# Kernel optimization log

Measured on AMD Instinct MI355X. Metric: run time of the kernel, lower is better.

The kernel has to match this reference:

```python
import jax, jax.numpy as jnp
import numpy as np
from jax import lax

NUM_UNITS = 128
INPUT_DIM = 128
NUM_STEPS = 512
BATCH = 256
FORGET_BIAS = 1.0  # BasicLSTMCell(num_units, 1.0)


def setup_inputs() -> dict:
    key = jax.random.key(0)
    k1, k2 = jax.random.split(key)
    x = jax.random.normal(k1, (BATCH, NUM_STEPS, INPUT_DIM), dtype=jnp.float32)
    # BasicLSTMCell kernel: [input_dim + num_units, 4*num_units], gate order i, j, f, o
    W = jax.random.normal(k2, (INPUT_DIM + NUM_UNITS, 4 * NUM_UNITS), dtype=jnp.float32) * 0.05
    b = jnp.zeros((4 * NUM_UNITS,), dtype=jnp.float32)  # zeros init in TF
    return {"x": x, "W": W, "b": b}


def reference(x, W, b):
    # x: [B, T, D]; faithful BasicLSTMCell recurrence, return_sequences=True
    B = x.shape[0]
    U = NUM_UNITS

    def step(carry, xt):
        c, h = carry
        gates = jnp.concatenate([xt, h], axis=-1) @ W + b  # [B, 4U]
        i, j, f, o = jnp.split(gates, 4, axis=-1)
        new_c = c * jax.nn.sigmoid(f + FORGET_BIAS) + jax.nn.sigmoid(i) * jnp.tanh(j)
        new_h = jnp.tanh(new_c) * jax.nn.sigmoid(o)
        return (new_c, new_h), new_h

    init = (jnp.zeros((B, U), x.dtype), jnp.zeros((B, U), x.dtype))
    _, hs = lax.scan(step, init, jnp.swapaxes(x, 0, 1))  # hs: [T, B, U]
    return jnp.swapaxes(hs, 0, 1)  # [B, T, U]
```

## Files before the change

### kernel.cpp

```cpp
#include <hip/hip_runtime.h>
#include <cstdint>

#define B_ 256
#define T_ 512
#define D_ 128
#define U_ 128

typedef _Float16 h2_t __attribute__((ext_vector_type(2)));
typedef _Float16 f16x4 __attribute__((ext_vector_type(4)));
typedef _Float16 f16x8 __attribute__((ext_vector_type(8)));
typedef float f32x4 __attribute__((ext_vector_type(4)));

static __device__ __forceinline__ uint32_t pack2(float a, float b) {
  h2_t h;
  h.x = (_Float16)a;
  h.y = (_Float16)b;
  return __builtin_bit_cast(uint32_t, h);
}
static __device__ __forceinline__ h2_t as_h2(uint32_t u) {
  return __builtin_bit_cast(h2_t, u);
}
static __device__ __forceinline__ float dot2acc(uint32_t a, uint32_t w, float acc) {
#if __has_builtin(__builtin_amdgcn_fdot2)
  return __builtin_amdgcn_fdot2(as_h2(a), as_h2(w), acc, false);
#else
  h2_t ha = as_h2(a), hw = as_h2(w);
  return acc + (float)ha.x * (float)hw.x + (float)ha.y * (float)hw.y;
#endif
}

static __device__ __forceinline__ float fexp2(float x) {
#if __has_builtin(__builtin_amdgcn_exp2f)
  return __builtin_amdgcn_exp2f(x);
#else
  return __exp2f(x);
#endif
}
static __device__ __forceinline__ float frcp(float x) {
#if __has_builtin(__builtin_amdgcn_rcpf)
  return __builtin_amdgcn_rcpf(x);
#else
  return __frcp_rn(x);
#endif
}
#define LOG2E_ 1.44269504f
static __device__ __forceinline__ float sigm(float v) {
  return frcp(1.0f + fexp2(-LOG2E_ * v));
}
static __device__ __forceinline__ float tanh_(float v) {
  float r = frcp(1.0f + fexp2(-2.0f * LOG2E_ * v));
  return __builtin_fmaf(2.0f, r, -1.0f);
}

__global__ __launch_bounds__(256) void wt_kernel(const float* __restrict__ W,
                                                 _Float16* __restrict__ Wtx,
                                                 _Float16* __restrict__ Wth) {
  int id = blockIdx.x * 256 + threadIdx.x;
  int col = id >> 8, k = id & 255;
  _Float16 v = (_Float16)W[(size_t)k * 512 + col];
  if (k < 128) Wtx[col * 128 + k] = v;
  else Wth[col * 128 + (k - 128)] = v;
}

__global__ __launch_bounds__(256, 2) void gx_kernel(const float* __restrict__ x,
                                                    const _Float16* __restrict__ Wt,
                                                    const float* __restrict__ bias,
                                                    _Float16* __restrict__ gx) {
  __shared__ __align__(16) _Float16 As[64 * 136];
  const int tid = threadIdx.x;
  const int w = tid >> 6, l = tid & 63;
  const size_t rowBase = (size_t)blockIdx.x * 64;

  const float4* xs = reinterpret_cast<const float4*>(x + rowBase * 128);
#pragma unroll
  for (int n = 0; n < 8; ++n) {
    int idx4 = tid + 256 * n;
    float4 v = xs[idx4];
    int f = idx4 * 4;
    int r = f >> 7, cc = f & 127;
    f16x4 p;
    p.x = (_Float16)v.x; p.y = (_Float16)v.y;
    p.z = (_Float16)v.z; p.w = (_Float16)v.w;
    *reinterpret_cast<f16x4*>(&As[r * 136 + cc]) = p;
  }
  __syncthreads();

  f16x8 af[4][4];
#pragma unroll
  for (int rt = 0; rt < 4; ++rt)
#pragma unroll
    for (int kk = 0; kk < 4; ++kk)
      af[rt][kk] = *reinterpret_cast<const f16x8*>(
          &As[(16 * rt + (l & 15)) * 136 + 32 * kk + 8 * (l >> 4)]);

  const int colBase = 128 * w;
#pragma unroll 1
  for (int ct = 0; ct < 8; ++ct) {
    const int col = colBase + 16 * ct + (l & 15);
    const float bb = bias[col] + ((col >= 256 && col < 384) ? 1.0f : 0.0f);
    f32x4 acc[4];
#pragma unroll
    for (int rt = 0; rt < 4; ++rt) acc[rt] = (f32x4){0.f, 0.f, 0.f, 0.f};
    const _Float16* wtc = Wt + (size_t)col * 128 + 8 * (l >> 4);
#pragma unroll
    for (int kk = 0; kk < 4; ++kk) {
      f16x8 bf = *reinterpret_cast<const f16x8*>(wtc + 32 * kk);
#pragma unroll
      for (int rt = 0; rt < 4; ++rt)
        acc[rt] = __builtin_amdgcn_mfma_f32_16x16x32_f16(af[rt][kk], bf, acc[rt], 0, 0, 0);
    }
    const int u = col & 127, g = col >> 7;
#pragma unroll
    for (int rt = 0; rt < 4; ++rt) {
      size_t row = rowBase + 16 * rt + 4 * (l >> 4);
#pragma unroll
      for (int j = 0; j < 4; ++j)
        gx[(row + j) * 512 + u * 4 + g] = (_Float16)(acc[rt][j] + bb);
    }
  }
}

__global__ __launch_bounds__(512, 1) void rec_kernel(
    const _Float16* __restrict__ Wth,
    const uint16_t* __restrict__ gx2,
    float* __restrict__ out) {
  __shared__ __align__(16) _Float16 hbuf[2][4][128];
  const int tid = threadIdx.x;
  const int b = blockIdx.x;
  const int w = tid >> 6, l = tid & 63;
  const int lq = l >> 4;
  const int u = 16 * w + (l & 15);
  const bool wr = (lq == 0);

  f16x8 bw[4][4];
#pragma unroll
  for (int g = 0; g < 4; ++g) {
    const _Float16* wc = Wth + (size_t)(128 * g + u) * 128 + 8 * lq;
#pragma unroll
    for (int kk = 0; kk < 4; ++kk)
      bw[g][kk] = *reinterpret_cast<const f16x8*>(wc + 32 * kk);
  }
#pragma unroll
  for (int g = 0; g < 4; ++g)
#pragma unroll
    for (int kk = 0; kk < 4; ++kk)
      asm volatile("" : "+a"(bw[g][kk]));

  const uint16_t* gxb = gx2 + (size_t)b * T_ * 512 + 4 * u;
  float* ob = out + (size_t)b * T_ * U_ + u;

  reinterpret_cast<uint32_t*>(&hbuf[0][0][0])[tid] = 0u;

  f32x4 Z = {0.f, 0.f, 0.f, 0.f};
  asm volatile("" : "+v"(Z));
  float cst = 0.0f;

#define GXLD(idx) \
  (*reinterpret_cast<const f16x4*>(gxb + (size_t)((idx) < T_ ? (idx) : (T_ - 1)) * 512))

  f16x4 gp0 = GXLD(0), gp1 = GXLD(1), gp2 = GXLD(2), gp3 = GXLD(3);
  __syncthreads();

#define MFMA_INIT(d, a, bfr)                                  \
  asm("v_mfma_f32_16x16x32_f16 %0, %1, %2, %3"                \
      : "=v"(d) : "v"(a), "a"(bfr), "v"(Z))
#define MFMA_ACC(d, a, bfr)                                   \
  asm("v_mfma_f32_16x16x32_f16 %0, %1, %2, %0"                \
      : "+v"(d) : "v"(a), "a"(bfr))

#define LDS_BARRIER()                                                  \
  do {                                                                 \
    asm volatile("s_waitcnt lgkmcnt(0)\n\ts_barrier" ::: "memory");    \
    __builtin_amdgcn_sched_barrier(0);                                 \
  } while (0)

#define STEP(tt, p, gv)                                                        \
  {                                                                            \
    const _Float16* hb = &hbuf[p][lq][0];                                      \
    f16x8 a0 = *reinterpret_cast<const f16x8*>(hb + 8 * lq);                   \
    f16x8 a1 = *reinterpret_cast<const f16x8*>(hb + 32 + 8 * lq);              \
    f16x8 a2 = *reinterpret_cast<const f16x8*>(hb + 64 + 8 * lq);              \
    f16x8 a3 = *reinterpret_cast<const f16x8*>(hb + 96 + 8 * lq);              \
    f32x4 c0, c1, c2, c3, d0, d1, d2, d3;                                      \
    MFMA_INIT(c0, a0, bw[0][0]);                                               \
    MFMA_INIT(c1, a0, bw[1][0]);                                               \
    MFMA_INIT(c2, a0, bw[2][0]);                                               \
    MFMA_INIT(c3, a0, bw[3][0]);                                               \
    MFMA_INIT(d0, a2, bw[0][2]);                                               \
    MFMA_INIT(d1, a2, bw[1][2]);                                               \
    MFMA_INIT(d2, a2, bw[2][2]);                                               \
    MFMA_INIT(d3, a2, bw[3][2]);                                               \
    MFMA_ACC(c0, a1, bw[0][1]);                                                \
    MFMA_ACC(c1, a1, bw[1][1]);                                                \
    MFMA_ACC(c2, a1, bw[2][1]);                                                \
    MFMA_ACC(c3, a1, bw[3][1]);                                                \
    MFMA_ACC(d0, a3, bw[0][3]);                                                \
    MFMA_ACC(d1, a3, bw[1][3]);                                                \
    MFMA_ACC(d2, a3, bw[2][3]);                                                \
    MFMA_ACC(d3, a3, bw[3][3]);                                                \
         \
    asm volatile("s_nop 7\n\ts_nop 7"                                          \
                 : "+v"(c0), "+v"(c1), "+v"(c2), "+v"(c3),                     \
                   "+v"(d0), "+v"(d1), "+v"(d2), "+v"(d3));                    \
    const float gi = (c0[0] + d0[0]) + (float)(gv).x;                          \
    const float gj = (c1[0] + d1[0]) + (float)(gv).y;                          \
    const float gf = (c2[0] + d2[0]) + (float)(gv).z;                          \
    const float go = (c3[0] + d3[0]) + (float)(gv).w;                          \
    cst = __builtin_fmaf(cst, sigm(gf), sigm(gi) * tanh_(gj));                 \
    const float hh = tanh_(cst) * sigm(go);                                    \
    hbuf[(p) ^ 1][lq][u] = (_Float16)hh;                                       \
    if (wr) ob[(size_t)(tt) * U_] = hh;                                        \
    LDS_BARRIER();                                                             \
  }

#pragma unroll 1
  for (int t = 0; t < T_; t += 4) {
    STEP(t + 0, 0, gp0)
    gp0 = GXLD(t + 4);
    STEP(t + 1, 1, gp1)
    gp1 = GXLD(t + 5);
    STEP(t + 2, 0, gp2)
    gp2 = GXLD(t + 6);
    STEP(t + 3, 1, gp3)
    gp3 = GXLD(t + 7);
  }
#undef STEP
#undef MFMA_INIT
#undef MFMA_ACC
#undef LDS_BARRIER
#undef GXLD
}

__global__ __launch_bounds__(512, 2) void lstm_fused_kernel(
    const float* __restrict__ x, const float* __restrict__ W,
    const float* __restrict__ bias, float* __restrict__ out) {
  __shared__ __align__(16) uint32_t a_lds[2][128];
  __shared__ float g_lds[512];
  const int tid = threadIdx.x;
  const int b = blockIdx.x;
  uint32_t wreg[128];
#pragma unroll
  for (int q4 = 0; q4 < 32; ++q4) {
    float f[8];
#pragma unroll
    for (int r = 0; r < 8; ++r) f[r] = W[(q4 * 8 + r) * 512 + tid];
#pragma unroll
    for (int rr = 0; rr < 4; ++rr)
      wreg[q4 * 4 + rr] = pack2(f[2 * rr], f[2 * rr + 1]);
  }
  const float bjv = bias[tid];
  const float* xb = x + (size_t)b * (T_ * D_);
  float* ob = out + (size_t)b * (T_ * U_);
  if (tid < 32) {
    float4 x4 = reinterpret_cast<const float4*>(xb)[tid];
    reinterpret_cast<uint2*>(&a_lds[0][0])[tid] =
        make_uint2(pack2(x4.x, x4.y), pack2(x4.z, x4.w));
  }
  if (tid >= 64 && tid < 128) a_lds[0][tid] = 0u;
  __syncthreads();
  float c = 0.0f;
  int p = 0;
  for (int t = 0; t < T_; ++t) {
    float4 xp;
    const bool pf = (tid < 32) && (t + 1 < T_);
    if (pf) xp = reinterpret_cast<const float4*>(xb + (t + 1) * D_)[tid];
    const uint4* av = reinterpret_cast<const uint4*>(&a_lds[p][0]);
    float a0 = bjv, a1 = 0.0f, a2 = 0.0f, a3 = 0.0f;
#pragma unroll
    for (int q = 0; q < 32; ++q) {
      uint4 a4 = av[q];
      a0 = dot2acc(a4.x, wreg[4 * q + 0], a0);
      a1 = dot2acc(a4.y, wreg[4 * q + 1], a1);
      a2 = dot2acc(a4.z, wreg[4 * q + 2], a2);
      a3 = dot2acc(a4.w, wreg[4 * q + 3], a3);
    }
    g_lds[tid] = (a0 + a1) + (a2 + a3);
    __syncthreads();
    if (tid < 128) {
      const float gi = g_lds[tid];
      const float gj = g_lds[128 + tid];
      const float gf = g_lds[256 + tid];
      const float go = g_lds[384 + tid];
      c = c * sigm(gf + 1.0f) + sigm(gi) * tanh_(gj);
      const float h = tanh_(c) * sigm(go);
      ob[t * U_ + tid] = h;
      reinterpret_cast<_Float16*>(&a_lds[p ^ 1][64])[tid] = (_Float16)h;
    }
    if (pf) {
      reinterpret_cast<uint2*>(&a_lds[p ^ 1][0])[tid] =
          make_uint2(pack2(xp.x, xp.y), pack2(xp.z, xp.w));
    }
    __syncthreads();
    p ^= 1;
  }
}

extern "C" void kernel_launch(void* const* d_in, const int* in_sizes, int n_in,
                              void* d_out, int out_size, void* d_ws, size_t ws_size,
                              hipStream_t stream) {
  (void)in_sizes; (void)n_in; (void)out_size;
  const float* x = (const float*)d_in[0];
  const float* W = (const float*)d_in[1];
  const float* b = (const float*)d_in[2];
  float* out = (float*)d_out;

  const size_t WTX_BYTES = (size_t)512 * 128 * 2;
  const size_t WTH_BYTES = (size_t)512 * 128 * 2;
  const size_t GX_BYTES = (size_t)B_ * T_ * 512 * 2;
  if (ws_size >= WTX_BYTES + WTH_BYTES + GX_BYTES) {
    _Float16* wtx = (_Float16*)d_ws;
    _Float16* wth = (_Float16*)((char*)d_ws + WTX_BYTES);
    _Float16* gxp = (_Float16*)((char*)d_ws + WTX_BYTES + WTH_BYTES);
    wt_kernel<<<512, 256, 0, stream>>>(W, wtx, wth);
    gx_kernel<<<2048, 256, 0, stream>>>(x, wtx, b, gxp);
    rec_kernel<<<256, 512, 0, stream>>>(wth, (const uint16_t*)gxp, out);
  } else {
    lstm_fused_kernel<<<256, 512, 0, stream>>>(x, W, b, out);
  }
}
```

Baseline: 305.9 us.

## Process four batch rows per recurrence block to cut grid from 256 to 64

The recurrent kernel now handles four batch elements per workgroup, one per lane quadrant, instead of one. Each step issues four sets of MFMAs over separate padded h buffers and picks each lane's gates with a select. This gives every lane useful output work and interleaves independent MFMA chains to hide latency. In exchange, each block does four times the MFMA work per step, and only 64 blocks run, which leaves most CUs idle.

```diff
diff --git a/kernel.cpp b/kernel.cpp
--- a/kernel.cpp
+++ b/kernel.cpp
@@ -50,6 +50,11 @@
 static __device__ __forceinline__ float tanh_(float v) {
   float r = frcp(1.0f + fexp2(-2.0f * LOG2E_ * v));
   return __builtin_fmaf(2.0f, r, -1.0f);
+}
+static __device__ __forceinline__ float sel4(float a, float b, float c, float d, int lq) {
+  float x = (lq & 1) ? b : a;
+  float y = (lq & 1) ? d : c;
+  return (lq & 2) ? y : x;
 }
 
 __global__ __launch_bounds__(256) void wt_kernel(const float* __restrict__ W,
@@ -124,13 +129,12 @@
     const _Float16* __restrict__ Wth,
     const uint16_t* __restrict__ gx2,
     float* __restrict__ out) {
-  __shared__ __align__(16) _Float16 hbuf[2][4][128];
+  __shared__ __align__(16) _Float16 hbuf[2][4 * 144];
   const int tid = threadIdx.x;
-  const int b = blockIdx.x;
   const int w = tid >> 6, l = tid & 63;
   const int lq = l >> 4;
   const int u = 16 * w + (l & 15);
-  const bool wr = (lq == 0);
+  const int b = blockIdx.x * 4 + lq;
 
   f16x8 bw[4][4];
 #pragma unroll
@@ -149,7 +153,8 @@
   const uint16_t* gxb = gx2 + (size_t)b * T_ * 512 + 4 * u;
   float* ob = out + (size_t)b * T_ * U_ + u;
 
-  reinterpret_cast<uint32_t*>(&hbuf[0][0][0])[tid] = 0u;
+  for (int i = tid; i < 576; i += 512)
+    reinterpret_cast<uint32_t*>(&hbuf[0][0])[i] = 0u;
 
   f32x4 Z = {0.f, 0.f, 0.f, 0.f};
   asm volatile("" : "+v"(Z));
@@ -158,14 +163,14 @@
 #define GXLD(idx) \
   (*reinterpret_cast<const f16x4*>(gxb + (size_t)((idx) < T_ ? (idx) : (T_ - 1)) * 512))
 
-  f16x4 gp0 = GXLD(0), gp1 = GXLD(1), gp2 = GXLD(2), gp3 = GXLD(3);
+  f16x4 gA = GXLD(0), gB = GXLD(1);
   __syncthreads();
 
-#define MFMA_INIT(d, a, bfr)                                  \
-  asm("v_mfma_f32_16x16x32_f16 %0, %1, %2, %3"                \
+#define MFMA_INIT(d, a, bfr)                    \
+  asm("v_mfma_f32_16x16x32_f16 %0, %1, %2, %3"  \
       : "=v"(d) : "v"(a), "a"(bfr), "v"(Z))
-#define MFMA_ACC(d, a, bfr)                                   \
-  asm("v_mfma_f32_16x16x32_f16 %0, %1, %2, %0"                \
+#define MFMA_ACC(d, a, bfr)                     \
+  asm("v_mfma_f32_16x16x32_f16 %0, %1, %2, %0"  \
       : "+v"(d) : "v"(a), "a"(bfr))
 
 #define LDS_BARRIER()                                                  \
@@ -174,60 +179,74 @@
     __builtin_amdgcn_sched_barrier(0);                                 \
   } while (0)
 
-#define STEP(tt, p, gv)                                                        \
+#define MF16(a0_, a1_, a2_, a3_, c0_, c1_, c2_, c3_, d0_, d1_, d2_, d3_) \
+  MFMA_INIT(c0_, a0_, bw[0][0]); MFMA_INIT(c1_, a0_, bw[1][0]);          \
+  MFMA_INIT(c2_, a0_, bw[2][0]); MFMA_INIT(c3_, a0_, bw[3][0]);          \
+  MFMA_INIT(d0_, a2_, bw[0][2]); MFMA_INIT(d1_, a2_, bw[1][2]);          \
+  MFMA_INIT(d2_, a2_, bw[2][2]); MFMA_INIT(d3_, a2_, bw[3][2]);          \
+  MFMA_ACC(c0_, a1_, bw[0][1]);  MFMA_ACC(c1_, a1_, bw[1][1]);           \
+  MFMA_ACC(c2_, a1_, bw[2][1]);  MFMA_ACC(c3_, a1_, bw[3][1]);           \
+  MFMA_ACC(d0_, a3_, bw[0][3]);  MFMA_ACC(d1_, a3_, bw[1][3]);           \
+  MFMA_ACC(d2_, a3_, bw[2][3]);  MFMA_ACC(d3_, a3_, bw[3][3]);
+
+#define EXTRACT(gi_, gj_, gf_, go_, c0_, c1_, c2_, c3_, d0_, d1_, d2_, d3_)    \
+  asm volatile("s_nop 7\n\ts_nop 7"                                            \
+               : "+v"(c0_), "+v"(c1_), "+v"(c2_), "+v"(c3_),                   \
+                 "+v"(d0_), "+v"(d1_), "+v"(d2_), "+v"(d3_));                  \
+  gi_ = c0_[0] + d0_[0]; gj_ = c1_[0] + d1_[0];                                \
+  gf_ = c2_[0] + d2_[0]; go_ = c3_[0] + d3_[0];
+
+#define LDH(hp, q, kk) \
+  (*reinterpret_cast<const f16x8*>((hp) + (q) * 144 + 32 * (kk) + 8 * lq))
+
+#define PERIOD(tt, p, gv)                                                      \
   {                                                                            \
-    const _Float16* hb = &hbuf[p][lq][0];                                      \
-    f16x8 a0 = *reinterpret_cast<const f16x8*>(hb + 8 * lq);                   \
-    f16x8 a1 = *reinterpret_cast<const f16x8*>(hb + 32 + 8 * lq);              \
-    f16x8 a2 = *reinterpret_cast<const f16x8*>(hb + 64 + 8 * lq);              \
-    f16x8 a3 = *reinterpret_cast<const f16x8*>(hb + 96 + 8 * lq);              \
-    f32x4 c0, c1, c2, c3, d0, d1, d2, d3;                                      \
-    MFMA_INIT(c0, a0, bw[0][0]);                                               \
-    MFMA_INIT(c1, a0, bw[1][0]);                                               \
-    MFMA_INIT(c2, a0, bw[2][0]);                                               \
-    MFMA_INIT(c3, a0, bw[3][0]);                                               \
-    MFMA_INIT(d0, a2, bw[0][2]);                                               \
-    MFMA_INIT(d1, a2, bw[1][2]);                                               \
-    MFMA_INIT(d2, a2, bw[2][2]);                                               \
-    MFMA_INIT(d3, a2, bw[3][2]);                                               \
-    MFMA_ACC(c0, a1, bw[0][1]);                                                \
-    MFMA_ACC(c1, a1, bw[1][1]);                                                \
-    MFMA_ACC(c2, a1, bw[2][1]);                                                \
-    MFMA_ACC(c3, a1, bw[3][1]);                                                \
-    MFMA_ACC(d0, a3, bw[0][3]);                                                \
-    MFMA_ACC(d1, a3, bw[1][3]);                                                \
-    MFMA_ACC(d2, a3, bw[2][3]);                                                \
-    MFMA_ACC(d3, a3, bw[3][3]);                                                \
-         \
-    asm volatile("s_nop 7\n\ts_nop 7"                                          \
-                 : "+v"(c0), "+v"(c1), "+v"(c2), "+v"(c3),                     \
-                   "+v"(d0), "+v"(d1), "+v"(d2), "+v"(d3));                    \
-    const float gi = (c0[0] + d0[0]) + (float)(gv).x;                          \
-    const float gj = (c1[0] + d1[0]) + (float)(gv).y;                          \
-    const float gf = (c2[0] + d2[0]) + (float)(gv).z;                          \
-    const float go = (c3[0] + d3[0]) + (float)(gv).w;                          \
+    const _Float16* hp = &hbuf[p][0];                                          \
+    f16x8 A00 = LDH(hp, 0, 0), A01 = LDH(hp, 0, 1),                            \
+          A02 = LDH(hp, 0, 2), A03 = LDH(hp, 0, 3);                            \
+    f16x8 A10 = LDH(hp, 1, 0), A11 = LDH(hp, 1, 1),                            \
+          A12 = LDH(hp, 1, 2), A13 = LDH(hp, 1, 3);                            \
+    f16x8 A20 = LDH(hp, 2, 0), A21 = LDH(hp, 2, 1),                            \
+          A22 = LDH(hp, 2, 2), A23 = LDH(hp, 2, 3);                            \
+    f16x8 A30 = LDH(hp, 3, 0), A31 = LDH(hp, 3, 1),                            \
+          A32 = LDH(hp, 3, 2), A33 = LDH(hp, 3, 3);                            \
+    f32x4 X0, X1, X2, X3, X4, X5, X6, X7;                                      \
+    f32x4 Y0, Y1, Y2, Y3, Y4, Y5, Y6, Y7;                                      \
+    float G0i, G0j, G0f, G0o, G1i, G1j, G1f, G1o;                              \
+    float G2i, G2j, G2f, G2o, G3i, G3j, G3f, G3o;                              \
+    MF16(A00, A01, A02, A03, X0, X1, X2, X3, X4, X5, X6, X7)                   \
+    MF16(A10, A11, A12, A13, Y0, Y1, Y2, Y3, Y4, Y5, Y6, Y7)                   \
+    EXTRACT(G0i, G0j, G0f, G0o, X0, X1, X2, X3, X4, X5, X6, X7)                \
+    MF16(A20, A21, A22, A23, X0, X1, X2, X3, X4, X5, X6, X7)                   \
+    EXTRACT(G1i, G1j, G1f, G1o, Y0, Y1, Y2, Y3, Y4, Y5, Y6, Y7)                \
+    MF16(A30, A31, A32, A33, Y0, Y1, Y2, Y3, Y4, Y5, Y6, Y7)                   \
+    EXTRACT(G2i, G2j, G2f, G2o, X0, X1, X2, X3, X4, X5, X6, X7)                \
+    EXTRACT(G3i, G3j, G3f, G3o, Y0, Y1, Y2, Y3, Y4, Y5, Y6, Y7)                \
+    float gi = sel4(G0i, G1i, G2i, G3i, lq) + (float)(gv).x;                   \
+    float gj = sel4(G0j, G1j, G2j, G3j, lq) + (float)(gv).y;                   \
+    float gf = sel4(G0f, G1f, G2f, G3f, lq) + (float)(gv).z;                   \
+    float go = sel4(G0o, G1o, G2o, G3o, lq) + (float)(gv).w;                   \
     cst = __builtin_fmaf(cst, sigm(gf), sigm(gi) * tanh_(gj));                 \
     const float hh = tanh_(cst) * sigm(go);                                    \
-    hbuf[(p) ^ 1][lq][u] = (_Float16)hh;                                       \
-    if (wr) ob[(size_t)(tt) * U_] = hh;                                        \
+    hbuf[(p) ^ 1][lq * 144 + u] = (_Float16)hh;                                \
+    ob[(size_t)(tt) * U_] = hh;                                                \
     LDS_BARRIER();                                                             \
   }
 
 #pragma unroll 1
-  for (int t = 0; t < T_; t += 4) {
-    STEP(t + 0, 0, gp0)
-    gp0 = GXLD(t + 4);
-    STEP(t + 1, 1, gp1)
-    gp1 = GXLD(t + 5);
-    STEP(t + 2, 0, gp2)
-    gp2 = GXLD(t + 6);
-    STEP(t + 3, 1, gp3)
-    gp3 = GXLD(t + 7);
-  }
-#undef STEP
+  for (int t = 0; t < T_; t += 2) {
+    PERIOD(t + 0, 0, gA)
+    gA = GXLD(t + 2);
+    PERIOD(t + 1, 1, gB)
+    gB = GXLD(t + 3);
+  }
+#undef PERIOD
+#undef LDH
+#undef EXTRACT
+#undef MF16
+#undef LDS_BARRIER
 #undef MFMA_INIT
 #undef MFMA_ACC
-#undef LDS_BARRIER
 #undef GXLD
 }
 
@@ -313,7 +332,7 @@
     _Float16* gxp = (_Float16*)((char*)d_ws + WTX_BYTES + WTH_BYTES);
     wt_kernel<<<512, 256, 0, stream>>>(W, wtx, wth);
     gx_kernel<<<2048, 256, 0, stream>>>(x, wtx, b, gxp);
-    rec_kernel<<<256, 512, 0, stream>>>(wth, (const uint16_t*)gxp, out);
+    rec_kernel<<<64, 512, 0, stream>>>(wth, (const uint16_t*)gxp, out);
   } else {
     lstm_fused_kernel<<<256, 512, 0, stream>>>(x, W, b, out);
   }
```

New measurement: 740.6 us. 142% more time.

## Halve recurrent block to 4 waves, each computing 32 units via 8 MFMA chains

Applied to the files above, without the earlier changes.

The recurrent kernel now runs 256 threads (4 waves) per batch row instead of 512. Each wave handles 32 hidden units, holding 8 weight fragment sets in AGPRs and issuing 32 MFMAs per step in 8 independent accumulation chains. The h buffer shrinks to a single shared row, and only the first quarter of each wave's lanes writes it. This cuts barrier participants and per-step LDS traffic, at the cost of longer per-wave MFMA chains and more register pressure on the serial critical path.

```diff
diff --git a/kernel.cpp b/kernel.cpp
--- a/kernel.cpp
+++ b/kernel.cpp
@@ -120,52 +120,59 @@
   }
 }
 
-__global__ __launch_bounds__(512, 1) void rec_kernel(
+__global__ __launch_bounds__(256, 1) void rec_kernel(
     const _Float16* __restrict__ Wth,
     const uint16_t* __restrict__ gx2,
     float* __restrict__ out) {
-  __shared__ __align__(16) _Float16 hbuf[2][4][128];
+  __shared__ __align__(16) _Float16 hbuf[2][128];
   const int tid = threadIdx.x;
   const int b = blockIdx.x;
   const int w = tid >> 6, l = tid & 63;
   const int lq = l >> 4;
-  const int u = 16 * w + (l & 15);
+  const int cI = l & 15;
   const bool wr = (lq == 0);
 
-  f16x8 bw[4][4];
-#pragma unroll
-  for (int g = 0; g < 4; ++g) {
-    const _Float16* wc = Wth + (size_t)(128 * g + u) * 128 + 8 * lq;
-#pragma unroll
-    for (int kk = 0; kk < 4; ++kk)
-      bw[g][kk] = *reinterpret_cast<const f16x8*>(wc + 32 * kk);
-  }
+  f16x8 bw[8][4];
 #pragma unroll
   for (int g = 0; g < 4; ++g)
 #pragma unroll
-    for (int kk = 0; kk < 4; ++kk)
-      asm volatile("" : "+a"(bw[g][kk]));
-
-  const uint16_t* gxb = gx2 + (size_t)b * T_ * 512 + 4 * u;
-  float* ob = out + (size_t)b * T_ * U_ + u;
-
-  reinterpret_cast<uint32_t*>(&hbuf[0][0][0])[tid] = 0u;
+    for (int s = 0; s < 2; ++s) {
+      const _Float16* wc =
+          Wth + (size_t)(128 * g + 32 * w + 16 * s + cI) * 128 + 8 * lq;
+#pragma unroll
+      for (int kt = 0; kt < 4; ++kt)
+        bw[g * 2 + s][kt] = *reinterpret_cast<const f16x8*>(wc + 32 * kt);
+    }
+#pragma unroll
+  for (int i = 0; i < 8; ++i)
+#pragma unroll
+    for (int kt = 0; kt < 4; ++kt)
+      asm volatile("" : "+a"(bw[i][kt]));
+
+  const int u0 = 32 * w + cI;
+  const uint16_t* gxb = gx2 + (size_t)b * T_ * 512 + 4 * u0;
+  float* ob = out + (size_t)b * T_ * U_ + u0;
+
+  if (tid < 128) reinterpret_cast<uint32_t*>(&hbuf[0][0])[tid] = 0u;
 
   f32x4 Z = {0.f, 0.f, 0.f, 0.f};
   asm volatile("" : "+v"(Z));
-  float cst = 0.0f;
-
-#define GXLD(idx) \
-  (*reinterpret_cast<const f16x4*>(gxb + (size_t)((idx) < T_ ? (idx) : (T_ - 1)) * 512))
-
-  f16x4 gp0 = GXLD(0), gp1 = GXLD(1), gp2 = GXLD(2), gp3 = GXLD(3);
+  float cst0 = 0.0f, cst1 = 0.0f;
+
+#define GXA(idx) (*reinterpret_cast<const f16x4*>( \
+    gxb + (size_t)((idx) < T_ ? (idx) : (T_ - 1)) * 512))
+#define GXB(idx) (*reinterpret_cast<const f16x4*>( \
+    gxb + (size_t)((idx) < T_ ? (idx) : (T_ - 1)) * 512 + 64))
+
+  f16x4 g0a = GXA(0), g0b = GXB(0), g1a = GXA(1), g1b = GXB(1);
+  f16x4 g2a = GXA(2), g2b = GXB(2), g3a = GXA(3), g3b = GXB(3);
   __syncthreads();
 
-#define MFMA_INIT(d, a, bfr)                                  \
-  asm("v_mfma_f32_16x16x32_f16 %0, %1, %2, %3"                \
+#define MFMA_INIT(d, a, bfr)                    \
+  asm("v_mfma_f32_16x16x32_f16 %0, %1, %2, %3"  \
       : "=v"(d) : "v"(a), "a"(bfr), "v"(Z))
-#define MFMA_ACC(d, a, bfr)                                   \
-  asm("v_mfma_f32_16x16x32_f16 %0, %1, %2, %0"                \
+#define MFMA_ACC(d, a, bfr)                     \
+  asm("v_mfma_f32_16x16x32_f16 %0, %1, %2, %0"  \
       : "+v"(d) : "v"(a), "a"(bfr))
 
 #define LDS_BARRIER()                                                  \
@@ -174,61 +181,72 @@
     __builtin_amdgcn_sched_barrier(0);                                 \
   } while (0)
 
-#define STEP(tt, p, gv)                                                        \
+#define STEP(tt, p, gva, gvb)                                                  \
   {                                                                            \
-    const _Float16* hb = &hbuf[p][lq][0];                                      \
+    const _Float16* hb = &hbuf[p][0];                                          \
     f16x8 a0 = *reinterpret_cast<const f16x8*>(hb + 8 * lq);                   \
     f16x8 a1 = *reinterpret_cast<const f16x8*>(hb + 32 + 8 * lq);              \
     f16x8 a2 = *reinterpret_cast<const f16x8*>(hb + 64 + 8 * lq);              \
     f16x8 a3 = *reinterpret_cast<const f16x8*>(hb + 96 + 8 * lq);              \
-    f32x4 c0, c1, c2, c3, d0, d1, d2, d3;                                      \
-    MFMA_INIT(c0, a0, bw[0][0]);                                               \
-    MFMA_INIT(c1, a0, bw[1][0]);                                               \
-    MFMA_INIT(c2, a0, bw[2][0]);                                               \
-    MFMA_INIT(c3, a0, bw[3][0]);                                               \
-    MFMA_INIT(d0, a2, bw[0][2]);                                               \
-    MFMA_INIT(d1, a2, bw[1][2]);                                               \
-    MFMA_INIT(d2, a2, bw[2][2]);                                               \
-    MFMA_INIT(d3, a2, bw[3][2]);                                               \
-    MFMA_ACC(c0, a1, bw[0][1]);                                                \
-    MFMA_ACC(c1, a1, bw[1][1]);                                                \
-    MFMA_ACC(c2, a1, bw[2][1]);                                                \
-    MFMA_ACC(c3, a1, bw[3][1]);                                                \
-    MFMA_ACC(d0, a3, bw[0][3]);                                                \
-    MFMA_ACC(d1, a3, bw[1][3]);                                                \
-    MFMA_ACC(d2, a3, bw[2][3]);                                                \
-    MFMA_ACC(d3, a3, bw[3][3]);                                                \
-         \
+    f32x4 q0, q1, q2, q3, q4, q5, q6, q7;                                      \
+    MFMA_INIT(q0, a0, bw[0][0]); MFMA_INIT(q1, a0, bw[1][0]);                  \
+    MFMA_INIT(q2, a0, bw[2][0]); MFMA_INIT(q3, a0, bw[3][0]);                  \
+    MFMA_INIT(q4, a0, bw[4][0]); MFMA_INIT(q5, a0, bw[5][0]);                  \
+    MFMA_INIT(q6, a0, bw[6][0]); MFMA_INIT(q7, a0, bw[7][0]);                  \
+    MFMA_ACC(q0, a1, bw[0][1]);  MFMA_ACC(q1, a1, bw[1][1]);                   \
+    MFMA_ACC(q2, a1, bw[2][1]);  MFMA_ACC(q3, a1, bw[3][1]);                   \
+    MFMA_ACC(q4, a1, bw[4][1]);  MFMA_ACC(q5, a1, bw[5][1]);                   \
+    MFMA_ACC(q6, a1, bw[6][1]);  MFMA_ACC(q7, a1, bw[7][1]);                   \
+    MFMA_ACC(q0, a2, bw[0][2]);  MFMA_ACC(q1, a2, bw[1][2]);                   \
+    MFMA_ACC(q2, a2, bw[2][2]);  MFMA_ACC(q3, a2, bw[3][2]);                   \
+    MFMA_ACC(q4, a2, bw[4][2]);  MFMA_ACC(q5, a2, bw[5][2]);                   \
+    MFMA_ACC(q6, a2, bw[6][2]);  MFMA_ACC(q7, a2, bw[7][2]);                   \
+    MFMA_ACC(q0, a3, bw[0][3]);  MFMA_ACC(q1, a3, bw[1][3]);                   \
+    MFMA_ACC(q2, a3, bw[2][3]);  MFMA_ACC(q3, a3, bw[3][3]);                   \
+    MFMA_ACC(q4, a3, bw[4][3]);  MFMA_ACC(q5, a3, bw[5][3]);                   \
+    MFMA_ACC(q6, a3, bw[6][3]);  MFMA_ACC(q7, a3, bw[7][3]);                   \
     asm volatile("s_nop 7\n\ts_nop 7"                                          \
-                 : "+v"(c0), "+v"(c1), "+v"(c2), "+v"(c3),                     \
-                   "+v"(d0), "+v"(d1), "+v"(d2), "+v"(d3));                    \
-    const float gi = (c0[0] + d0[0]) + (float)(gv).x;                          \
-    const float gj = (c1[0] + d1[0]) + (float)(gv).y;                          \
-    const float gf = (c2[0] + d2[0]) + (float)(gv).z;                          \
-    const float go = (c3[0] + d3[0]) + (float)(gv).w;                          \
-    cst = __builtin_fmaf(cst, sigm(gf), sigm(gi) * tanh_(gj));                 \
-    const float hh = tanh_(cst) * sigm(go);                                    \
-    hbuf[(p) ^ 1][lq][u] = (_Float16)hh;                                       \
-    if (wr) ob[(size_t)(tt) * U_] = hh;                                        \
+                 : "+v"(q0), "+v"(q1), "+v"(q2), "+v"(q3),                     \
+                   "+v"(q4), "+v"(q5), "+v"(q6), "+v"(q7));                    \
+        \
+    const float gi0 = q0[0] + (float)(gva).x;                                  \
+    const float gj0 = q2[0] + (float)(gva).y;                                  \
+    const float gf0 = q4[0] + (float)(gva).z;                                  \
+    const float go0 = q6[0] + (float)(gva).w;                                  \
+    const float gi1 = q1[0] + (float)(gvb).x;                                  \
+    const float gj1 = q3[0] + (float)(gvb).y;                                  \
+    const float gf1 = q5[0] + (float)(gvb).z;                                  \
+    const float go1 = q7[0] + (float)(gvb).w;                                  \
+    cst0 = __builtin_fmaf(cst0, sigm(gf0), sigm(gi0) * tanh_(gj0));            \
+    cst1 = __builtin_fmaf(cst1, sigm(gf1), sigm(gi1) * tanh_(gj1));            \
+    const float h0 = tanh_(cst0) * sigm(go0);                                  \
+    const float h1 = tanh_(cst1) * sigm(go1);                                  \
+    if (wr) {                                                                  \
+      hbuf[(p) ^ 1][u0] = (_Float16)h0;                                        \
+      hbuf[(p) ^ 1][u0 + 16] = (_Float16)h1;                                   \
+      ob[(size_t)(tt) * U_] = h0;                                              \
+      ob[(size_t)(tt) * U_ + 16] = h1;                                         \
+    }                                                                          \
     LDS_BARRIER();                                                             \
   }
 
 #pragma unroll 1
   for (int t = 0; t < T_; t += 4) {
-    STEP(t + 0, 0, gp0)
-    gp0 = GXLD(t + 4);
-    STEP(t + 1, 1, gp1)
-    gp1 = GXLD(t + 5);
-    STEP(t + 2, 0, gp2)
-    gp2 = GXLD(t + 6);
-    STEP(t + 3, 1, gp3)
-    gp3 = GXLD(t + 7);
+    STEP(t + 0, 0, g0a, g0b)
+    g0a = GXA(t + 4); g0b = GXB(t + 4);
+    STEP(t + 1, 1, g1a, g1b)
+    g1a = GXA(t + 5); g1b = GXB(t + 5);
+    STEP(t + 2, 0, g2a, g2b)
+    g2a = GXA(t + 6); g2b = GXB(t + 6);
+    STEP(t + 3, 1, g3a, g3b)
+    g3a = GXA(t + 7); g3b = GXB(t + 7);
   }
 #undef STEP
+#undef LDS_BARRIER
 #undef MFMA_INIT
 #undef MFMA_ACC
-#undef LDS_BARRIER
-#undef GXLD
+#undef GXA
+#undef GXB
 }
 
 __global__ __launch_bounds__(512, 2) void lstm_fused_kernel(
@@ -313,7 +331,7 @@
     _Float16* gxp = (_Float16*)((char*)d_ws + WTX_BYTES + WTH_BYTES);
     wt_kernel<<<512, 256, 0, stream>>>(W, wtx, wth);
     gx_kernel<<<2048, 256, 0, stream>>>(x, wtx, b, gxp);
-    rec_kernel<<<256, 512, 0, stream>>>(wth, (const uint16_t*)gxp, out);
+    rec_kernel<<<256, 256, 0, stream>>>(wth, (const uint16_t*)gxp, out);
   } else {
     lstm_fused_kernel<<<256, 512, 0, stream>>>(x, W, b, out);
   }
```

Result: slower. 348.6 us (+14.0%).
